# Performance work log

Measured on AMD Instinct MI355X. Metric: run time of the kernel, lower is better.

Reference implementation:

```python
import jax, jax.numpy as jnp
import numpy as np


def _wn(v, g):
    # weight-norm: w[o, i] = g[o] * v[o, i] / ||v[o, :]||
    return g[:, None] * v / jnp.linalg.norm(v, axis=1, keepdims=True)


def setup_inputs() -> dict:
    key = jax.random.key(0)
    ks = jax.random.split(key, 8)
    B, C, H, W = 16, 512, 64, 64
    K, D = 2048, 64
    return {
        "z": jax.random.normal(ks[0], (B, C, H, W), dtype=jnp.float32),
        "codebook": jax.random.normal(ks[1], (K, D), dtype=jnp.float32),
        "in_v": jax.random.normal(ks[2], (D, C), dtype=jnp.float32),
        "in_g": jax.random.uniform(ks[3], (D,), dtype=jnp.float32, minval=0.5, maxval=1.5),
        "in_b": jax.random.normal(ks[4], (D,), dtype=jnp.float32) * 0.02,
        "out_v": jax.random.normal(ks[5], (C, D), dtype=jnp.float32),
        "out_g": jax.random.uniform(ks[6], (C,), dtype=jnp.float32, minval=0.5, maxval=1.5),
        "out_b": jax.random.normal(ks[7], (C,), dtype=jnp.float32) * 0.02,
    }


def reference(z, codebook, in_v, in_g, in_b, out_v, out_g, out_b):
    COMMIT_W = 0.25
    B, C, H, W = z.shape
    D = codebook.shape[1]

    Wi = _wn(in_v, in_g)    # [D, C]
    Wo = _wn(out_v, out_g)  # [C, D]

    # in_proj (1x1 conv): b c h w -> b d h w
    z_e = jnp.einsum('bchw,dc->bdhw', z, Wi) + in_b[None, :, None, None]

    # flatten tokens: (b h w) d
    z_e_flat = z_e.transpose(0, 2, 3, 1).reshape(-1, D)

    dist = (jnp.sum(z_e_flat * z_e_flat, axis=1, keepdims=True)
            - 2.0 * z_e_flat @ codebook.T
            + jnp.sum(codebook * codebook, axis=1)[None, :])
    indices_flat = jnp.argmin(dist, axis=1)            # [(BHW)]
    indices = indices_flat.reshape(B, H, W)

    z_q_flat = codebook[indices_flat]                  # gather [(BHW), D]
    z_q = z_q_flat.reshape(B, H, W, D).transpose(0, 3, 1, 2)  # b d h w

    sg = jax.lax.stop_gradient
    commitment_loss = jnp.mean((sg(z_e) - z_q) ** 2)
    codebook_loss = jnp.mean((sg(z_q) - z_e) ** 2)
    vq_loss = codebook_loss + COMMIT_W * commitment_loss

    # straight-through
    z_q_st = z_e + sg(z_q - z_e)

    # out_proj (1x1 conv): b d h w -> b c h w
    out = jnp.einsum('bdhw,cd->bchw', z_q_st, Wo) + out_b[None, :, None, None]
    return out, indices, vq_loss
```

## Files before the change

### kernel.cpp

```cpp
#include <hip/hip_runtime.h>
#include <math.h>


typedef __attribute__((address_space(1))) const unsigned int* gas_ptr;
typedef __attribute__((address_space(3))) unsigned int* las_ptr;
#define GLD_LDS16(gsrc, ldst) \
  __builtin_amdgcn_global_load_lds((gas_ptr)(const void*)(gsrc), \
                                   (las_ptr)(void*)(ldst), 16, 0, 0)


__global__ void k_prep_wi(const float* __restrict__ v, const float* __restrict__ g,
                          float* __restrict__ wiT){
  const int d = blockIdx.x;
  const int tid = threadIdx.x;
  float s = 0.f;
  for (int c = tid; c < 512; c += 256){ float x = v[d*512+c]; s = fmaf(x,x,s); }
  __shared__ float red[4];
  #pragma unroll
  for (int o = 32; o > 0; o >>= 1) s += __shfl_down(s, o);
  if ((tid & 63) == 0) red[tid >> 6] = s;
  __syncthreads();
  const float nrm = sqrtf(red[0]+red[1]+red[2]+red[3]);
  const float gd = g[d];
  for (int c = tid; c < 512; c += 256) wiT[c*64 + d] = gd * v[d*512+c] / nrm;
}

__global__ void k_prep_wo(const float* __restrict__ v, const float* __restrict__ g,
                          float* __restrict__ wot){
  const int c = blockIdx.x;
  const int d = threadIdx.x;
  const float x = v[c*64+d];
  float s = x*x;
  #pragma unroll
  for (int o = 32; o > 0; o >>= 1) s += __shfl_down(s, o);
  const float nrm = __shfl(sqrtf(s), 0);
  wot[d*512 + c] = g[c] * x / nrm;
}

__global__ void k_table(const float* __restrict__ cbk, const float* __restrict__ wot,
                        const float* __restrict__ ob, float* __restrict__ table,
                        float* __restrict__ ne, float* __restrict__ cbm2T){
  const int k = blockIdx.x;
  const int tid = threadIdx.x;
  __shared__ float e[64];
  if (tid < 64) e[tid] = cbk[k*64 + tid];
  __syncthreads();
  if (tid < 64){
    float x = e[tid];
    cbm2T[tid*2048 + k] = -2.0f * x;
    float s = x*x;
    #pragma unroll
    for (int o = 32; o > 0; o >>= 1) s += __shfl_down(s, o);
    if (tid == 0) ne[k] = s;
  }
  const int c = tid;
  float acc = ob[c];
  #pragma unroll 16
  for (int d = 0; d < 64; d++) acc = fmaf(e[d], wot[d*512 + c], acc);
  table[(size_t)k*512 + c] = acc;
}

__global__ __launch_bounds__(256, 1) void k_inproj(
    const float* __restrict__ z, const float* __restrict__ wiT,
    const float* __restrict__ inb, float* __restrict__ ze)
{
  __shared__ __align__(16) float z_s[16*256];
  __shared__ __align__(16) float wi_s[16*68];
  const int tid = threadIdx.x;
  const int T0  = blockIdx.x << 8;
  const int b   = T0 >> 12;
  const int hw0 = T0 & 4095;
  const float* zb = z + ((size_t)b << 21) + hw0;

  const int tgp = tid & 31;
  const int dgp = tid >> 5;
  const int ccb = tid >> 6;
  const int c64 = tid & 63;

  float acc[8][8];
  #pragma unroll
  for (int i = 0; i < 8; i++)
    #pragma unroll
    for (int j = 0; j < 8; j++) acc[i][j] = 0.f;

  float4 pz[4]; float pw[4];
  #pragma unroll
  for (int q = 0; q < 4; q++){
    pz[q] = *(const float4*)(zb + (size_t)(ccb + 4*q) * 4096 + c64*4);
    pw[q] = wiT[(ccb + 4*q)*64 + c64];
  }
  #pragma unroll
  for (int q = 0; q < 4; q++){
    *(float4*)&z_s[(ccb + 4*q)*256 + c64*4] = pz[q];
    wi_s[(ccb + 4*q)*68 + c64] = pw[q];
  }
  __syncthreads();

  for (int c0 = 0;;){
    const int nxt = c0 + 16;
    if (nxt < 512){
      #pragma unroll
      for (int q = 0; q < 4; q++){
        pz[q] = *(const float4*)(zb + (size_t)(nxt + ccb + 4*q) * 4096 + c64*4);
        pw[q] = wiT[(nxt + ccb + 4*q)*64 + c64];
      }
    }
    #pragma unroll 4
    for (int cc = 0; cc < 16; cc++){
      const float4 ta = *(const float4*)&z_s[cc*256 + tgp*4];
      const float4 tb = *(const float4*)&z_s[cc*256 + 128 + tgp*4];
      const float4 w0 = *(const float4*)&wi_s[cc*68 + dgp*8];
      const float4 w1 = *(const float4*)&wi_s[cc*68 + dgp*8 + 4];
      const float tv[8] = {ta.x,ta.y,ta.z,ta.w, tb.x,tb.y,tb.z,tb.w};
      const float wv[8] = {w0.x,w0.y,w0.z,w0.w, w1.x,w1.y,w1.z,w1.w};
      #pragma unroll
      for (int i = 0; i < 8; i++)
        #pragma unroll
        for (int j = 0; j < 8; j++)
          acc[i][j] = fmaf(tv[j], wv[i], acc[i][j]);
    }
    if (nxt >= 512) break;
    __syncthreads();
    #pragma unroll
    for (int q = 0; q < 4; q++){
      *(float4*)&z_s[(ccb + 4*q)*256 + c64*4] = pz[q];
      wi_s[(ccb + 4*q)*68 + c64] = pw[q];
    }
    __syncthreads();
    c0 = nxt;
  }

  #pragma unroll
  for (int i = 0; i < 8; i++){
    const int d = dgp*8 + i;
    const float bd = inb[d];
    float4 o0 = {acc[i][0]+bd, acc[i][1]+bd, acc[i][2]+bd, acc[i][3]+bd};
    float4 o1 = {acc[i][4]+bd, acc[i][5]+bd, acc[i][6]+bd, acc[i][7]+bd};
    *(float4*)(ze + (size_t)d*65536 + T0 + tgp*4)       = o0;
    *(float4*)(ze + (size_t)d*65536 + T0 + 128 + tgp*4) = o1;
  }
}

__global__ __launch_bounds__(256, 2) void k_main3(
    const float* __restrict__ ze, const float* __restrict__ cbm2T,
    const float* __restrict__ cbk, const float* __restrict__ ne,
    const float* __restrict__ table, float* __restrict__ out,
    float* __restrict__ oidx, double* __restrict__ loss)
{
  __shared__ __align__(16) float ze_s[64*128];
  __shared__ __align__(16) float cb_s[2][8*272];
  __shared__ int bidx_s[128];

  const int tid = threadIdx.x;
  const int t0  = blockIdx.x << 7;
  const int b   = t0 >> 12;
  const int hw0 = t0 & 4095;
  const int w   = tid >> 6;
  const int l4  = (tid & 63) << 2;

  #pragma unroll
  for (int j = 0; j < 8; j++){
    const int idx = tid + 256*j;
    const int row = idx >> 5, col4 = idx & 31;
    *(float4*)&ze_s[row*128 + col4*4] =
        *(const float4*)(ze + (size_t)row*65536 + t0 + col4*4);
  }

  const int tg = tid & 15;
  const int kg = tid >> 4;
  float best[8]; int bidx[8];
  #pragma unroll
  for (int j = 0; j < 8; j++){ best[j] = INFINITY; bidx[j] = 0; }

  {
    const float* gb = cbm2T + (size_t)(2*w)*2048 + l4;
    GLD_LDS16(gb,        &cb_s[0][(2*w)  *272]);
    GLD_LDS16(gb + 2048, &cb_s[0][(2*w+1)*272]);
  }
  __syncthreads();

  float acc[8][16];
  for (int s = 0; s < 64; s++){
    const int buf = s & 1;
    const int dq = s & 7, kc = (s >> 3) << 8;
    if (s < 63){
      const int s1 = s + 1;
      const int ndq = s1 & 7, nkc = (s1 >> 3) << 8;
      const float* gb = cbm2T + (size_t)(ndq*8 + 2*w)*2048 + nkc + l4;
      GLD_LDS16(gb,        &cb_s[buf^1][(2*w)  *272]);
      GLD_LDS16(gb + 2048, &cb_s[buf^1][(2*w+1)*272]);
    }
    if (dq == 0){
      #pragma unroll
      for (int q = 0; q < 4; q++){
        const float4 nv = *(const float4*)&ne[kc + kg*16 + q*4];
        const float nn[4] = {nv.x, nv.y, nv.z, nv.w};
        #pragma unroll
        for (int r = 0; r < 4; r++)
          #pragma unroll
          for (int j = 0; j < 8; j++) acc[j][q*4+r] = nn[r];
      }
    }
    const int dbase = dq << 3;
    #pragma unroll
    for (int d = 0; d < 8; d++){
      const int dr = dbase + d;
      const float4 za = *(const float4*)&ze_s[dr*128 + tg*4];
      const float4 zb = *(const float4*)&ze_s[dr*128 + 64 + tg*4];
      const float4 c0 = *(const float4*)&cb_s[buf][d*272 + kg*16];
      const float4 c1 = *(const float4*)&cb_s[buf][d*272 + kg*16 + 4];
      const float4 c2 = *(const float4*)&cb_s[buf][d*272 + kg*16 + 8];
      const float4 c3 = *(const float4*)&cb_s[buf][d*272 + kg*16 + 12];
      const float zz[8]  = {za.x,za.y,za.z,za.w, zb.x,zb.y,zb.z,zb.w};
      const float cv[16] = {c0.x,c0.y,c0.z,c0.w, c1.x,c1.y,c1.z,c1.w,
                            c2.x,c2.y,c2.z,c2.w, c3.x,c3.y,c3.z,c3.w};
      #pragma unroll
      for (int j = 0; j < 8; j++)
        #pragma unroll
        for (int i = 0; i < 16; i++)
          acc[j][i] = fmaf(zz[j], cv[i], acc[j][i]);
    }
    if (dq == 7){
      #pragma unroll
      for (int i = 0; i < 16; i++){
        const int k = kc + kg*16 + i;
        #pragma unroll
        for (int j = 0; j < 8; j++)
          if (acc[j][i] < best[j]){ best[j] = acc[j][i]; bidx[j] = k; }
      }
    }
    __syncthreads();
  }

  float* rb = &cb_s[0][0];
  int*   ri = (int*)(&cb_s[0][0] + 2048);
  #pragma unroll
  for (int j = 0; j < 8; j++){
    const int t = (j < 4) ? (tg*4 + j) : (64 + tg*4 + (j - 4));
    rb[t*16 + kg] = best[j];
    ri[t*16 + kg] = bidx[j];
  }
  __syncthreads();

  float myloss = 0.f;
  if (tid < 128){
    const int t = tid;
    float bv = rb[t*16]; int bi = ri[t*16];
    #pragma unroll
    for (int q = 1; q < 16; q++){
      const float vq = rb[t*16 + q]; const int iq = ri[t*16 + q];
      if (vq < bv || (vq == bv && iq < bi)){ bv = vq; bi = iq; }
    }
    bidx_s[t] = bi;
    oidx[t0 + t] = (float)bi;
    const float* e = cbk + (size_t)bi * 64;
    #pragma unroll 8
    for (int d = 0; d < 64; d++){
      const float diff = ze_s[d*128 + t] - e[d];
      myloss = fmaf(diff, diff, myloss);
    }
  }
  #pragma unroll
  for (int o = 32; o > 0; o >>= 1) myloss += __shfl_down(myloss, o);
  if (tid < 128 && (tid & 63) == 0) atomicAdd(loss, (double)myloss);
  __syncthreads();

  {
    const int tl = tid & 127, cg = tid >> 7;
    const int myk = bidx_s[tl];
    const float* trow = table + ((size_t)myk << 9) + cg*256;
    float* ob = out + (((size_t)b) << 21) + hw0 + tl;
    #pragma unroll 4
    for (int ci = 0; ci < 64; ci++){
      const float4 v = *(const float4*)(trow + ci*4);
      const size_t cbase = (size_t)(cg*256 + ci*4) << 12;
      ob[cbase        ] = v.x;
      ob[cbase +  4096] = v.y;
      ob[cbase +  8192] = v.z;
      ob[cbase + 12288] = v.w;
    }
  }
}

__global__ void k_finish(const double* __restrict__ loss, float* __restrict__ oloss){
  *oloss = (float)(1.25 * (*loss) / 4194304.0);
}


extern "C" void kernel_launch(void* const* d_in, const int* in_sizes, int n_in,
                              void* d_out, int out_size, void* d_ws, size_t ws_size,
                              hipStream_t stream) {
  const float* z   = (const float*)d_in[0];
  const float* cbk = (const float*)d_in[1];
  const float* inv = (const float*)d_in[2];
  const float* ing = (const float*)d_in[3];
  const float* inb = (const float*)d_in[4];
  const float* ov  = (const float*)d_in[5];
  const float* og  = (const float*)d_in[6];
  const float* ob  = (const float*)d_in[7];

  float* ws    = (float*)d_ws;
  float* wiT   = ws;
  float* wot   = ws + 32768;
  float* table = ws + 65536;
  float* ne    = ws + 65536 + 1048576;
  double* loss = (double*)(ws + 1116160);
  float* cbm2T = ws + 1179648;
  float* zebuf = ws + 2097152;

  float* out   = (float*)d_out;
  float* oidx  = out + 33554432;
  float* oloss = out + 33619968;

  hipMemsetAsync(loss, 0, sizeof(double), stream);
  k_prep_wi<<<64, 256, 0, stream>>>(inv, ing, wiT);
  k_prep_wo<<<512, 64, 0, stream>>>(ov, og, wot);
  k_table<<<2048, 512, 0, stream>>>(cbk, wot, ob, table, ne, cbm2T);
  k_inproj<<<256, 256, 0, stream>>>(z, wiT, inb, zebuf);
  k_main3<<<512, 256, 0, stream>>>(zebuf, cbm2T, cbk, ne, table, out, oidx, loss);
  k_finish<<<1, 1, 0, stream>>>(loss, oloss);
}
```

Measured before the change: 348.2 us.

## Fuse in-projection into main VQ kernel with 64-token tiles

Merges the separate in-projection kernel into the distance/argmin/output kernel, so z_e is computed into shared memory per block instead of written to and reread from a global buffer. Tiles shrink from 128 to 64 tokens per block, with smaller accumulator arrays and a higher occupancy target (4 blocks per CU, 1024 blocks in total), and z/weight tiles are streamed through async global-to-LDS loads. The trade-off is that each block reloads the whole codebook for half as many tokens, doubling codebook traffic and per-token sync overhead.

```diff
diff --git a/kernel.cpp b/kernel.cpp
--- a/kernel.cpp
+++ b/kernel.cpp
@@ -60,135 +60,96 @@
   table[(size_t)k*512 + c] = acc;
 }
 
-__global__ __launch_bounds__(256, 1) void k_inproj(
+__global__ __launch_bounds__(256, 4) void k_main(
     const float* __restrict__ z, const float* __restrict__ wiT,
-    const float* __restrict__ inb, float* __restrict__ ze)
-{
-  __shared__ __align__(16) float z_s[16*256];
-  __shared__ __align__(16) float wi_s[16*68];
-  const int tid = threadIdx.x;
-  const int T0  = blockIdx.x << 8;
-  const int b   = T0 >> 12;
-  const int hw0 = T0 & 4095;
-  const float* zb = z + ((size_t)b << 21) + hw0;
-
-  const int tgp = tid & 31;
-  const int dgp = tid >> 5;
-  const int ccb = tid >> 6;
-  const int c64 = tid & 63;
-
-  float acc[8][8];
-  #pragma unroll
-  for (int i = 0; i < 8; i++)
-    #pragma unroll
-    for (int j = 0; j < 8; j++) acc[i][j] = 0.f;
-
-  float4 pz[4]; float pw[4];
-  #pragma unroll
-  for (int q = 0; q < 4; q++){
-    pz[q] = *(const float4*)(zb + (size_t)(ccb + 4*q) * 4096 + c64*4);
-    pw[q] = wiT[(ccb + 4*q)*64 + c64];
-  }
-  #pragma unroll
-  for (int q = 0; q < 4; q++){
-    *(float4*)&z_s[(ccb + 4*q)*256 + c64*4] = pz[q];
-    wi_s[(ccb + 4*q)*68 + c64] = pw[q];
-  }
-  __syncthreads();
-
-  for (int c0 = 0;;){
-    const int nxt = c0 + 16;
-    if (nxt < 512){
-      #pragma unroll
-      for (int q = 0; q < 4; q++){
-        pz[q] = *(const float4*)(zb + (size_t)(nxt + ccb + 4*q) * 4096 + c64*4);
-        pw[q] = wiT[(nxt + ccb + 4*q)*64 + c64];
-      }
-    }
-    #pragma unroll 4
-    for (int cc = 0; cc < 16; cc++){
-      const float4 ta = *(const float4*)&z_s[cc*256 + tgp*4];
-      const float4 tb = *(const float4*)&z_s[cc*256 + 128 + tgp*4];
-      const float4 w0 = *(const float4*)&wi_s[cc*68 + dgp*8];
-      const float4 w1 = *(const float4*)&wi_s[cc*68 + dgp*8 + 4];
-      const float tv[8] = {ta.x,ta.y,ta.z,ta.w, tb.x,tb.y,tb.z,tb.w};
-      const float wv[8] = {w0.x,w0.y,w0.z,w0.w, w1.x,w1.y,w1.z,w1.w};
-      #pragma unroll
-      for (int i = 0; i < 8; i++)
-        #pragma unroll
-        for (int j = 0; j < 8; j++)
-          acc[i][j] = fmaf(tv[j], wv[i], acc[i][j]);
-    }
-    if (nxt >= 512) break;
-    __syncthreads();
-    #pragma unroll
-    for (int q = 0; q < 4; q++){
-      *(float4*)&z_s[(ccb + 4*q)*256 + c64*4] = pz[q];
-      wi_s[(ccb + 4*q)*68 + c64] = pw[q];
-    }
-    __syncthreads();
-    c0 = nxt;
-  }
-
-  #pragma unroll
-  for (int i = 0; i < 8; i++){
-    const int d = dgp*8 + i;
-    const float bd = inb[d];
-    float4 o0 = {acc[i][0]+bd, acc[i][1]+bd, acc[i][2]+bd, acc[i][3]+bd};
-    float4 o1 = {acc[i][4]+bd, acc[i][5]+bd, acc[i][6]+bd, acc[i][7]+bd};
-    *(float4*)(ze + (size_t)d*65536 + T0 + tgp*4)       = o0;
-    *(float4*)(ze + (size_t)d*65536 + T0 + 128 + tgp*4) = o1;
-  }
-}
-
-__global__ __launch_bounds__(256, 2) void k_main3(
-    const float* __restrict__ ze, const float* __restrict__ cbm2T,
+    const float* __restrict__ inb, const float* __restrict__ cbm2T,
     const float* __restrict__ cbk, const float* __restrict__ ne,
     const float* __restrict__ table, float* __restrict__ out,
     float* __restrict__ oidx, double* __restrict__ loss)
 {
-  __shared__ __align__(16) float ze_s[64*128];
-  __shared__ __align__(16) float cb_s[2][8*272];
-  __shared__ int bidx_s[128];
-
-  const int tid = threadIdx.x;
-  const int t0  = blockIdx.x << 7;
-  const int b   = t0 >> 12;
-  const int hw0 = t0 & 4095;
-  const int w   = tid >> 6;
-  const int l4  = (tid & 63) << 2;
-
-  #pragma unroll
-  for (int j = 0; j < 8; j++){
-    const int idx = tid + 256*j;
-    const int row = idx >> 5, col4 = idx & 31;
-    *(float4*)&ze_s[row*128 + col4*4] =
-        *(const float4*)(ze + (size_t)row*65536 + t0 + col4*4);
-  }
-
-  const int tg = tid & 15;
-  const int kg = tid >> 4;
-  float best[8]; int bidx[8];
-  #pragma unroll
-  for (int j = 0; j < 8; j++){ best[j] = INFINITY; bidx[j] = 0; }
+  __shared__ __align__(16) float ze_s[64*68];
+  __shared__ __align__(16) float rgb[2*2176];
+  __shared__ int bidx_s[64];
+
+  const int tid  = threadIdx.x;
+  const int w    = tid >> 6;
+  const int lane = tid & 63;
+  const int t0   = blockIdx.x << 6;
+  const int b    = t0 >> 12;
+  const int hw0  = t0 & 4095;
+  const float* zb = z + ((size_t)b << 21) + hw0;
+
+  const int tg  = tid & 15;
+  const int dgp = tid >> 4;
+
+  const int srow = w*4 + (lane >> 4);
+  const int scol = (lane & 15) << 2;
+
+  float acc1[4][4];
+  #pragma unroll
+  for (int i = 0; i < 4; i++)
+    #pragma unroll
+    for (int j = 0; j < 4; j++) acc1[i][j] = 0.f;
+
+  GLD_LDS16(zb + (size_t)srow*4096 + scol,  &rgb[0*2176 + w*256]);
+  GLD_LDS16(wiT + srow*64 + scol,           &rgb[0*2176 + 1024 + w*256]);
+  __syncthreads();
+
+  for (int c = 0; c < 32; c++){
+    const int buf = c & 1;
+    if (c < 31){
+      const int c0n = (c+1) << 4;
+      GLD_LDS16(zb + (size_t)(c0n + srow)*4096 + scol, &rgb[(buf^1)*2176 + w*256]);
+      GLD_LDS16(wiT + (c0n + srow)*64 + scol,          &rgb[(buf^1)*2176 + 1024 + w*256]);
+    }
+    const float* zc = &rgb[buf*2176];
+    const float* wc = &rgb[buf*2176 + 1024];
+    #pragma unroll 4
+    for (int cc = 0; cc < 16; cc++){
+      const float4 ta = *(const float4*)&zc[cc*64 + tg*4];
+      const float4 wv = *(const float4*)&wc[cc*64 + dgp*4];
+      const float tv[4] = {ta.x, ta.y, ta.z, ta.w};
+      const float wvv[4] = {wv.x, wv.y, wv.z, wv.w};
+      #pragma unroll
+      for (int i = 0; i < 4; i++)
+        #pragma unroll
+        for (int j = 0; j < 4; j++)
+          acc1[i][j] = fmaf(tv[j], wvv[i], acc1[i][j]);
+    }
+    __syncthreads();
+  }
+
+  #pragma unroll
+  for (int i = 0; i < 4; i++){
+    const int d = dgp*4 + i;
+    const float bd = inb[d];
+    float4 o = {acc1[i][0]+bd, acc1[i][1]+bd, acc1[i][2]+bd, acc1[i][3]+bd};
+    *(float4*)&ze_s[d*68 + tg*4] = o;
+  }
+  __syncthreads();
+
+  const int kg = dgp;
+  float best[4]; int bidx[4];
+  #pragma unroll
+  for (int j = 0; j < 4; j++){ best[j] = INFINITY; bidx[j] = 0; }
 
   {
-    const float* gb = cbm2T + (size_t)(2*w)*2048 + l4;
-    GLD_LDS16(gb,        &cb_s[0][(2*w)  *272]);
-    GLD_LDS16(gb + 2048, &cb_s[0][(2*w+1)*272]);
-  }
-  __syncthreads();
-
-  float acc[8][16];
+    const float* gbs = cbm2T + (size_t)(2*w)*2048 + lane*4;
+    GLD_LDS16(gbs,        &rgb[0*2176 + (2*w)  *272]);
+    GLD_LDS16(gbs + 2048, &rgb[0*2176 + (2*w+1)*272]);
+  }
+  __syncthreads();
+
+  float acc[4][16];
   for (int s = 0; s < 64; s++){
     const int buf = s & 1;
     const int dq = s & 7, kc = (s >> 3) << 8;
     if (s < 63){
       const int s1 = s + 1;
       const int ndq = s1 & 7, nkc = (s1 >> 3) << 8;
-      const float* gb = cbm2T + (size_t)(ndq*8 + 2*w)*2048 + nkc + l4;
-      GLD_LDS16(gb,        &cb_s[buf^1][(2*w)  *272]);
-      GLD_LDS16(gb + 2048, &cb_s[buf^1][(2*w+1)*272]);
+      const float* gbs = cbm2T + (size_t)(ndq*8 + 2*w)*2048 + nkc + lane*4;
+      GLD_LDS16(gbs,        &rgb[(buf^1)*2176 + (2*w)  *272]);
+      GLD_LDS16(gbs + 2048, &rgb[(buf^1)*2176 + (2*w+1)*272]);
     }
     if (dq == 0){
       #pragma unroll
@@ -198,24 +159,24 @@
         #pragma unroll
         for (int r = 0; r < 4; r++)
           #pragma unroll
-          for (int j = 0; j < 8; j++) acc[j][q*4+r] = nn[r];
+          for (int j = 0; j < 4; j++) acc[j][q*4+r] = nn[r];
       }
     }
+    const float* cbf = &rgb[buf*2176];
     const int dbase = dq << 3;
     #pragma unroll
     for (int d = 0; d < 8; d++){
       const int dr = dbase + d;
-      const float4 za = *(const float4*)&ze_s[dr*128 + tg*4];
-      const float4 zb = *(const float4*)&ze_s[dr*128 + 64 + tg*4];
-      const float4 c0 = *(const float4*)&cb_s[buf][d*272 + kg*16];
-      const float4 c1 = *(const float4*)&cb_s[buf][d*272 + kg*16 + 4];
-      const float4 c2 = *(const float4*)&cb_s[buf][d*272 + kg*16 + 8];
-      const float4 c3 = *(const float4*)&cb_s[buf][d*272 + kg*16 + 12];
-      const float zz[8]  = {za.x,za.y,za.z,za.w, zb.x,zb.y,zb.z,zb.w};
+      const float4 za = *(const float4*)&ze_s[dr*68 + tg*4];
+      const float4 c0 = *(const float4*)&cbf[d*272 + kg*16];
+      const float4 c1 = *(const float4*)&cbf[d*272 + kg*16 + 4];
+      const float4 c2 = *(const float4*)&cbf[d*272 + kg*16 + 8];
+      const float4 c3 = *(const float4*)&cbf[d*272 + kg*16 + 12];
+      const float zz[4]  = {za.x, za.y, za.z, za.w};
       const float cv[16] = {c0.x,c0.y,c0.z,c0.w, c1.x,c1.y,c1.z,c1.w,
                             c2.x,c2.y,c2.z,c2.w, c3.x,c3.y,c3.z,c3.w};
       #pragma unroll
-      for (int j = 0; j < 8; j++)
+      for (int j = 0; j < 4; j++)
         #pragma unroll
         for (int i = 0; i < 16; i++)
           acc[j][i] = fmaf(zz[j], cv[i], acc[j][i]);
@@ -225,25 +186,24 @@
       for (int i = 0; i < 16; i++){
         const int k = kc + kg*16 + i;
         #pragma unroll
-        for (int j = 0; j < 8; j++)
+        for (int j = 0; j < 4; j++)
           if (acc[j][i] < best[j]){ best[j] = acc[j][i]; bidx[j] = k; }
       }
     }
     __syncthreads();
   }
 
-  float* rb = &cb_s[0][0];
-  int*   ri = (int*)(&cb_s[0][0] + 2048);
-  #pragma unroll
-  for (int j = 0; j < 8; j++){
-    const int t = (j < 4) ? (tg*4 + j) : (64 + tg*4 + (j - 4));
+  float* rb = rgb;
+  int*   ri = (int*)(rgb + 1024);
+  #pragma unroll
+  for (int j = 0; j < 4; j++){
+    const int t = tg*4 + j;
     rb[t*16 + kg] = best[j];
     ri[t*16 + kg] = bidx[j];
   }
   __syncthreads();
 
-  float myloss = 0.f;
-  if (tid < 128){
+  if (tid < 64){
     const int t = tid;
     float bv = rb[t*16]; int bi = ri[t*16];
     #pragma unroll
@@ -253,27 +213,28 @@
     }
     bidx_s[t] = bi;
     oidx[t0 + t] = (float)bi;
+    float myloss = 0.f;
     const float* e = cbk + (size_t)bi * 64;
     #pragma unroll 8
     for (int d = 0; d < 64; d++){
-      const float diff = ze_s[d*128 + t] - e[d];
+      const float diff = ze_s[d*68 + t] - e[d];
       myloss = fmaf(diff, diff, myloss);
     }
-  }
-  #pragma unroll
-  for (int o = 32; o > 0; o >>= 1) myloss += __shfl_down(myloss, o);
-  if (tid < 128 && (tid & 63) == 0) atomicAdd(loss, (double)myloss);
+    #pragma unroll
+    for (int o = 32; o > 0; o >>= 1) myloss += __shfl_down(myloss, o);
+    if (t == 0) atomicAdd(loss, (double)myloss);
+  }
   __syncthreads();
 
   {
-    const int tl = tid & 127, cg = tid >> 7;
+    const int tl = tid & 63, cg = tid >> 6;
     const int myk = bidx_s[tl];
-    const float* trow = table + ((size_t)myk << 9) + cg*256;
+    const float* trow = table + ((size_t)myk << 9) + cg*128;
     float* ob = out + (((size_t)b) << 21) + hw0 + tl;
     #pragma unroll 4
-    for (int ci = 0; ci < 64; ci++){
+    for (int ci = 0; ci < 32; ci++){
       const float4 v = *(const float4*)(trow + ci*4);
-      const size_t cbase = (size_t)(cg*256 + ci*4) << 12;
+      const size_t cbase = (size_t)(cg*128 + ci*4) << 12;
       ob[cbase        ] = v.x;
       ob[cbase +  4096] = v.y;
       ob[cbase +  8192] = v.z;
@@ -306,7 +267,6 @@
   float* ne    = ws + 65536 + 1048576;
   double* loss = (double*)(ws + 1116160);
   float* cbm2T = ws + 1179648;
-  float* zebuf = ws + 2097152;
 
   float* out   = (float*)d_out;
   float* oidx  = out + 33554432;
@@ -316,7 +276,6 @@
   k_prep_wi<<<64, 256, 0, stream>>>(inv, ing, wiT);
   k_prep_wo<<<512, 64, 0, stream>>>(ov, og, wot);
   k_table<<<2048, 512, 0, stream>>>(cbk, wot, ob, table, ne, cbm2T);
-  k_inproj<<<256, 256, 0, stream>>>(z, wiT, inb, zebuf);
-  k_main3<<<512, 256, 0, stream>>>(zebuf, cbm2T, cbk, ne, table, out, oidx, loss);
+  k_main<<<1024, 256, 0, stream>>>(z, wiT, inb, cbm2T, cbk, ne, table, out, oidx, loss);
   k_finish<<<1, 1, 0, stream>>>(loss, oloss);
 }
```

Result: slower. 385.7 us (+10.8%).

## Split codebook argmin into quarter-codebook scan blocks plus a merge kernel

Applied to the files above, without the earlier changes.

The fused distance/argmin/output kernel is replaced by two kernels. The first runs 4096 blocks, each holding a 512-entry quarter of the codebook in LDS and scanning 64 tokens, and writes a per-quarter best candidate. The second merges the four candidates, computes the loss, and scatters the precomputed output-table rows. The goal is more parallelism and less streaming of the codebook per block. In exchange it adds a kernel launch, candidate traffic through global memory, a large LDS footprint limiting occupancy to one block, and a re-read of z_e from global memory in the merge.

```diff
diff --git a/kernel.cpp b/kernel.cpp
--- a/kernel.cpp
+++ b/kernel.cpp
@@ -1,12 +1,6 @@
 #include <hip/hip_runtime.h>
 #include <math.h>
 
-
-typedef __attribute__((address_space(1))) const unsigned int* gas_ptr;
-typedef __attribute__((address_space(3))) unsigned int* las_ptr;
-#define GLD_LDS16(gsrc, ldst) \
-  __builtin_amdgcn_global_load_lds((gas_ptr)(const void*)(gsrc), \
-                                   (las_ptr)(void*)(ldst), 16, 0, 0)
 
 
 __global__ void k_prep_wi(const float* __restrict__ v, const float* __restrict__ g,
@@ -141,139 +135,154 @@
   }
 }
 
-__global__ __launch_bounds__(256, 2) void k_main3(
-    const float* __restrict__ ze, const float* __restrict__ cbm2T,
-    const float* __restrict__ cbk, const float* __restrict__ ne,
+__global__ __launch_bounds__(256, 1) void k_scan(
+    const float* __restrict__ zebuf, const float* __restrict__ cbm2T,
+    const float* __restrict__ ne, float* __restrict__ candv,
+    int* __restrict__ candi)
+{
+  __shared__ __align__(16) float cb_s[32*1044];
+  __shared__ __align__(16) float ze_s[64*68];
+  const int tid = threadIdx.x;
+  const int q  = blockIdx.x & 3;
+  const int t0 = (blockIdx.x >> 2) << 6;
+
+  {
+    const float* src = cbm2T + (q << 9);
+    for (int m = 0; m < 32; m++){
+      const int g = m*1024 + tid*4;
+      const int d = g >> 9, kcol = g & 511;
+      const float4 v = *(const float4*)(src + d*2048 + kcol);
+      *(float4*)&cb_s[(kcol >> 4)*1044 + d*16 + (kcol & 15)] = v;
+    }
+  }
+  {
+    const int r0 = tid >> 4, c4 = (tid & 15) << 2;
+    #pragma unroll
+    for (int m = 0; m < 4; m++){
+      const int d = r0 + m*16;
+      *(float4*)&ze_s[d*68 + c4] =
+          *(const float4*)(zebuf + (size_t)d*65536 + t0 + c4);
+    }
+  }
+  __syncthreads();
+
+  const int tg = tid & 7;
+  const int kg = tid >> 3;
+  const int kbase = (q << 9) + (kg << 4);
+
+  float acc[8][16];
+  #pragma unroll
+  for (int i4 = 0; i4 < 4; i4++){
+    const float4 nv = *(const float4*)&ne[kbase + i4*4];
+    #pragma unroll
+    for (int j = 0; j < 8; j++){
+      acc[j][i4*4  ] = nv.x; acc[j][i4*4+1] = nv.y;
+      acc[j][i4*4+2] = nv.z; acc[j][i4*4+3] = nv.w;
+    }
+  }
+
+#define P8(CV, I) \
+  acc[0][I]=fmaf(za.x ,CV,acc[0][I]); acc[1][I]=fmaf(za.y ,CV,acc[1][I]); \
+  acc[2][I]=fmaf(za.z ,CV,acc[2][I]); acc[3][I]=fmaf(za.w ,CV,acc[3][I]); \
+  acc[4][I]=fmaf(zb4.x,CV,acc[4][I]); acc[5][I]=fmaf(zb4.y,CV,acc[5][I]); \
+  acc[6][I]=fmaf(zb4.z,CV,acc[6][I]); acc[7][I]=fmaf(zb4.w,CV,acc[7][I]);
+
+  const float* cbr = &cb_s[kg*1044];
+  #pragma unroll 2
+  for (int d = 0; d < 64; d++){
+    const float4 za  = *(const float4*)&ze_s[d*68 + tg*8];
+    const float4 zb4 = *(const float4*)&ze_s[d*68 + tg*8 + 4];
+    const float4 c0 = *(const float4*)(cbr + d*16);
+    const float4 c1 = *(const float4*)(cbr + d*16 + 4);
+    const float4 c2 = *(const float4*)(cbr + d*16 + 8);
+    const float4 c3 = *(const float4*)(cbr + d*16 + 12);
+    P8(c0.x, 0)  P8(c0.y, 1)  P8(c0.z, 2)  P8(c0.w, 3)
+    P8(c1.x, 4)  P8(c1.y, 5)  P8(c1.z, 6)  P8(c1.w, 7)
+    P8(c2.x, 8)  P8(c2.y, 9)  P8(c2.z,10)  P8(c2.w,11)
+    P8(c3.x,12)  P8(c3.y,13)  P8(c3.z,14)  P8(c3.w,15)
+  }
+#undef P8
+
+  float best[8]; int bidx[8];
+  #pragma unroll
+  for (int j = 0; j < 8; j++){ best[j] = INFINITY; bidx[j] = 0; }
+  #pragma unroll
+  for (int i = 0; i < 16; i++){
+    const int k = kbase + i;
+    #pragma unroll
+    for (int j = 0; j < 8; j++)
+      if (acc[j][i] < best[j]){ best[j] = acc[j][i]; bidx[j] = k; }
+  }
+
+  __syncthreads();
+  float* rb = cb_s;
+  int*   ri = (int*)(cb_s + 2048);
+  #pragma unroll
+  for (int j = 0; j < 8; j++){
+    const int t = tg*8 + j;
+    rb[t*32 + kg] = best[j];
+    ri[t*32 + kg] = bidx[j];
+  }
+  __syncthreads();
+
+  if (tid < 64){
+    const int t = tid;
+    float bv = rb[t*32]; int bi = ri[t*32];
+    #pragma unroll
+    for (int kk = 1; kk < 32; kk++){
+      const float vq = rb[t*32 + kk]; const int iq = ri[t*32 + kk];
+      if (vq < bv || (vq == bv && iq < bi)){ bv = vq; bi = iq; }
+    }
+    candv[(q << 16) + t0 + t] = bv;
+    candi[(q << 16) + t0 + t] = bi;
+  }
+}
+
+__global__ __launch_bounds__(256) void k_merge(
+    const float* __restrict__ candv, const int* __restrict__ candi,
+    const float* __restrict__ zebuf, const float* __restrict__ cbk,
     const float* __restrict__ table, float* __restrict__ out,
     float* __restrict__ oidx, double* __restrict__ loss)
 {
-  __shared__ __align__(16) float ze_s[64*128];
-  __shared__ __align__(16) float cb_s[2][8*272];
-  __shared__ int bidx_s[128];
-
-  const int tid = threadIdx.x;
-  const int t0  = blockIdx.x << 7;
+  __shared__ int bidx_s[64];
+  const int tid = threadIdx.x;
+  const int t0  = blockIdx.x << 6;
   const int b   = t0 >> 12;
   const int hw0 = t0 & 4095;
-  const int w   = tid >> 6;
-  const int l4  = (tid & 63) << 2;
-
-  #pragma unroll
-  for (int j = 0; j < 8; j++){
-    const int idx = tid + 256*j;
-    const int row = idx >> 5, col4 = idx & 31;
-    *(float4*)&ze_s[row*128 + col4*4] =
-        *(const float4*)(ze + (size_t)row*65536 + t0 + col4*4);
-  }
-
-  const int tg = tid & 15;
-  const int kg = tid >> 4;
-  float best[8]; int bidx[8];
-  #pragma unroll
-  for (int j = 0; j < 8; j++){ best[j] = INFINITY; bidx[j] = 0; }
-
-  {
-    const float* gb = cbm2T + (size_t)(2*w)*2048 + l4;
-    GLD_LDS16(gb,        &cb_s[0][(2*w)  *272]);
-    GLD_LDS16(gb + 2048, &cb_s[0][(2*w+1)*272]);
-  }
-  __syncthreads();
-
-  float acc[8][16];
-  for (int s = 0; s < 64; s++){
-    const int buf = s & 1;
-    const int dq = s & 7, kc = (s >> 3) << 8;
-    if (s < 63){
-      const int s1 = s + 1;
-      const int ndq = s1 & 7, nkc = (s1 >> 3) << 8;
-      const float* gb = cbm2T + (size_t)(ndq*8 + 2*w)*2048 + nkc + l4;
-      GLD_LDS16(gb,        &cb_s[buf^1][(2*w)  *272]);
-      GLD_LDS16(gb + 2048, &cb_s[buf^1][(2*w+1)*272]);
-    }
-    if (dq == 0){
-      #pragma unroll
-      for (int q = 0; q < 4; q++){
-        const float4 nv = *(const float4*)&ne[kc + kg*16 + q*4];
-        const float nn[4] = {nv.x, nv.y, nv.z, nv.w};
-        #pragma unroll
-        for (int r = 0; r < 4; r++)
-          #pragma unroll
-          for (int j = 0; j < 8; j++) acc[j][q*4+r] = nn[r];
-      }
-    }
-    const int dbase = dq << 3;
-    #pragma unroll
-    for (int d = 0; d < 8; d++){
-      const int dr = dbase + d;
-      const float4 za = *(const float4*)&ze_s[dr*128 + tg*4];
-      const float4 zb = *(const float4*)&ze_s[dr*128 + 64 + tg*4];
-      const float4 c0 = *(const float4*)&cb_s[buf][d*272 + kg*16];
-      const float4 c1 = *(const float4*)&cb_s[buf][d*272 + kg*16 + 4];
-      const float4 c2 = *(const float4*)&cb_s[buf][d*272 + kg*16 + 8];
-      const float4 c3 = *(const float4*)&cb_s[buf][d*272 + kg*16 + 12];
-      const float zz[8]  = {za.x,za.y,za.z,za.w, zb.x,zb.y,zb.z,zb.w};
-      const float cv[16] = {c0.x,c0.y,c0.z,c0.w, c1.x,c1.y,c1.z,c1.w,
-                            c2.x,c2.y,c2.z,c2.w, c3.x,c3.y,c3.z,c3.w};
-      #pragma unroll
-      for (int j = 0; j < 8; j++)
-        #pragma unroll
-        for (int i = 0; i < 16; i++)
-          acc[j][i] = fmaf(zz[j], cv[i], acc[j][i]);
-    }
-    if (dq == 7){
-      #pragma unroll
-      for (int i = 0; i < 16; i++){
-        const int k = kc + kg*16 + i;
-        #pragma unroll
-        for (int j = 0; j < 8; j++)
-          if (acc[j][i] < best[j]){ best[j] = acc[j][i]; bidx[j] = k; }
-      }
-    }
-    __syncthreads();
-  }
-
-  float* rb = &cb_s[0][0];
-  int*   ri = (int*)(&cb_s[0][0] + 2048);
-  #pragma unroll
-  for (int j = 0; j < 8; j++){
-    const int t = (j < 4) ? (tg*4 + j) : (64 + tg*4 + (j - 4));
-    rb[t*16 + kg] = best[j];
-    ri[t*16 + kg] = bidx[j];
-  }
-  __syncthreads();
-
-  float myloss = 0.f;
-  if (tid < 128){
+
+  if (tid < 64){
     const int t = tid;
-    float bv = rb[t*16]; int bi = ri[t*16];
-    #pragma unroll
-    for (int q = 1; q < 16; q++){
-      const float vq = rb[t*16 + q]; const int iq = ri[t*16 + q];
-      if (vq < bv || (vq == bv && iq < bi)){ bv = vq; bi = iq; }
+    float bv = candv[t0 + t]; int bi = candi[t0 + t];
+    #pragma unroll
+    for (int qq = 1; qq < 4; qq++){
+      const float vq = candv[(qq << 16) + t0 + t];
+      const int   iq = candi[(qq << 16) + t0 + t];
+      if (vq < bv){ bv = vq; bi = iq; }
     }
     bidx_s[t] = bi;
     oidx[t0 + t] = (float)bi;
+    float myloss = 0.f;
     const float* e = cbk + (size_t)bi * 64;
     #pragma unroll 8
     for (int d = 0; d < 64; d++){
-      const float diff = ze_s[d*128 + t] - e[d];
+      const float diff = zebuf[(size_t)d*65536 + t0 + t] - e[d];
       myloss = fmaf(diff, diff, myloss);
     }
-  }
-  #pragma unroll
-  for (int o = 32; o > 0; o >>= 1) myloss += __shfl_down(myloss, o);
-  if (tid < 128 && (tid & 63) == 0) atomicAdd(loss, (double)myloss);
+    #pragma unroll
+    for (int o = 32; o > 0; o >>= 1) myloss += __shfl_down(myloss, o);
+    if (t == 0) atomicAdd(loss, (double)myloss);
+  }
   __syncthreads();
 
   {
-    const int tl = tid & 127, cg = tid >> 7;
+    const int tl = tid & 63, cg = tid >> 6;
     const int myk = bidx_s[tl];
-    const float* trow = table + ((size_t)myk << 9) + cg*256;
+    const float* trow = table + ((size_t)myk << 9) + cg*128;
     float* ob = out + (((size_t)b) << 21) + hw0 + tl;
     #pragma unroll 4
-    for (int ci = 0; ci < 64; ci++){
+    for (int ci = 0; ci < 32; ci++){
       const float4 v = *(const float4*)(trow + ci*4);
-      const size_t cbase = (size_t)(cg*256 + ci*4) << 12;
+      const size_t cbase = (size_t)(cg*128 + ci*4) << 12;
       ob[cbase        ] = v.x;
       ob[cbase +  4096] = v.y;
       ob[cbase +  8192] = v.z;
@@ -303,10 +312,12 @@
   float* wiT   = ws;
   float* wot   = ws + 32768;
   float* table = ws + 65536;
-  float* ne    = ws + 65536 + 1048576;
+  float* ne    = ws + 1114112;
   double* loss = (double*)(ws + 1116160);
   float* cbm2T = ws + 1179648;
   float* zebuf = ws + 2097152;
+  float* candv = ws + 6291456;
+  int*   candi = (int*)(ws + 6553600);
 
   float* out   = (float*)d_out;
   float* oidx  = out + 33554432;
@@ -317,6 +328,7 @@
   k_prep_wo<<<512, 64, 0, stream>>>(ov, og, wot);
   k_table<<<2048, 512, 0, stream>>>(cbk, wot, ob, table, ne, cbm2T);
   k_inproj<<<256, 256, 0, stream>>>(z, wiT, inb, zebuf);
-  k_main3<<<512, 256, 0, stream>>>(zebuf, cbm2T, cbk, ne, table, out, oidx, loss);
+  k_scan<<<4096, 256, 0, stream>>>(zebuf, cbm2T, ne, candv, candi);
+  k_merge<<<1024, 256, 0, stream>>>(candv, candi, zebuf, cbk, table, out, oidx, loss);
   k_finish<<<1, 1, 0, stream>>>(loss, oloss);
 }
```

After: 496.5 us. +42.6%, slower.

## Deepen codebook prefetch to distance two with one barrier per step

Applied to the files above, without the earlier changes.

The main distance kernel now uses four LDS buffers for codebook slices and prefetches two steps ahead. It uses explicit vmcnt waits with a single raw s_barrier per step in place of the trailing __syncthreads. The codebook norms are staged into LDS once instead of being read from global memory each chunk, and the FMA loop runs at raised wave priority. The aim is to hide global-to-LDS latency and cut barrier stalls, at the cost of more LDS per block (which may affect occupancy) and hand-tuned waitcnt logic that must stay in step with the outstanding loads.

```diff
diff --git a/kernel.cpp b/kernel.cpp
--- a/kernel.cpp
+++ b/kernel.cpp
@@ -141,14 +141,15 @@
   }
 }
 
-__global__ __launch_bounds__(256, 2) void k_main3(
+__global__ __launch_bounds__(256, 2) void k_main4(
     const float* __restrict__ ze, const float* __restrict__ cbm2T,
     const float* __restrict__ cbk, const float* __restrict__ ne,
     const float* __restrict__ table, float* __restrict__ out,
     float* __restrict__ oidx, double* __restrict__ loss)
 {
   __shared__ __align__(16) float ze_s[64*128];
-  __shared__ __align__(16) float cb_s[2][8*272];
+  __shared__ __align__(16) float cb_s[4][8*272];
+  __shared__ __align__(16) float ne_s[2048];
   __shared__ int bidx_s[128];
 
   const int tid = threadIdx.x;
@@ -172,28 +173,43 @@
   #pragma unroll
   for (int j = 0; j < 8; j++){ best[j] = INFINITY; bidx[j] = 0; }
 
+  GLD_LDS16(ne + w*512 + l4,        &ne_s[w*512]);
+  GLD_LDS16(ne + w*512 + 256 + l4,  &ne_s[w*512 + 256]);
   {
     const float* gb = cbm2T + (size_t)(2*w)*2048 + l4;
     GLD_LDS16(gb,        &cb_s[0][(2*w)  *272]);
     GLD_LDS16(gb + 2048, &cb_s[0][(2*w+1)*272]);
   }
+  {
+    const float* gb = cbm2T + (size_t)(1*8 + 2*w)*2048 + l4;
+    GLD_LDS16(gb,        &cb_s[1][(2*w)  *272]);
+    GLD_LDS16(gb + 2048, &cb_s[1][(2*w+1)*272]);
+  }
   __syncthreads();
 
   float acc[8][16];
   for (int s = 0; s < 64; s++){
-    const int buf = s & 1;
+    const int buf = s & 3;
     const int dq = s & 7, kc = (s >> 3) << 8;
-    if (s < 63){
-      const int s1 = s + 1;
-      const int ndq = s1 & 7, nkc = (s1 >> 3) << 8;
+    if (s < 62){
+      const int s2 = s + 2;
+      const int ndq = s2 & 7, nkc = (s2 >> 3) << 8;
       const float* gb = cbm2T + (size_t)(ndq*8 + 2*w)*2048 + nkc + l4;
-      GLD_LDS16(gb,        &cb_s[buf^1][(2*w)  *272]);
-      GLD_LDS16(gb + 2048, &cb_s[buf^1][(2*w+1)*272]);
-    }
+      GLD_LDS16(gb,        &cb_s[s2 & 3][(2*w)  *272]);
+      GLD_LDS16(gb + 2048, &cb_s[s2 & 3][(2*w+1)*272]);
+      asm volatile("s_waitcnt vmcnt(4)" ::: "memory");
+    } else if (s == 62){
+      asm volatile("s_waitcnt vmcnt(2)" ::: "memory");
+    } else {
+      asm volatile("s_waitcnt vmcnt(0)" ::: "memory");
+    }
+    __builtin_amdgcn_s_barrier();
+    __builtin_amdgcn_sched_barrier(0);
+
     if (dq == 0){
       #pragma unroll
       for (int q = 0; q < 4; q++){
-        const float4 nv = *(const float4*)&ne[kc + kg*16 + q*4];
+        const float4 nv = *(const float4*)&ne_s[kc + kg*16 + q*4];
         const float nn[4] = {nv.x, nv.y, nv.z, nv.w};
         #pragma unroll
         for (int r = 0; r < 4; r++)
@@ -202,6 +218,7 @@
       }
     }
     const int dbase = dq << 3;
+    __builtin_amdgcn_s_setprio(1);
     #pragma unroll
     for (int d = 0; d < 8; d++){
       const int dr = dbase + d;
@@ -220,6 +237,7 @@
         for (int i = 0; i < 16; i++)
           acc[j][i] = fmaf(zz[j], cv[i], acc[j][i]);
     }
+    __builtin_amdgcn_s_setprio(0);
     if (dq == 7){
       #pragma unroll
       for (int i = 0; i < 16; i++){
@@ -229,8 +247,8 @@
           if (acc[j][i] < best[j]){ best[j] = acc[j][i]; bidx[j] = k; }
       }
     }
-    __syncthreads();
-  }
+  }
+  __syncthreads();
 
   float* rb = &cb_s[0][0];
   int*   ri = (int*)(&cb_s[0][0] + 2048);
@@ -303,7 +321,7 @@
   float* wiT   = ws;
   float* wot   = ws + 32768;
   float* table = ws + 65536;
-  float* ne    = ws + 65536 + 1048576;
+  float* ne    = ws + 1114112;
   double* loss = (double*)(ws + 1116160);
   float* cbm2T = ws + 1179648;
   float* zebuf = ws + 2097152;
@@ -317,6 +335,6 @@
   k_prep_wo<<<512, 64, 0, stream>>>(ov, og, wot);
   k_table<<<2048, 512, 0, stream>>>(cbk, wot, ob, table, ne, cbm2T);
   k_inproj<<<256, 256, 0, stream>>>(z, wiT, inb, zebuf);
-  k_main3<<<512, 256, 0, stream>>>(zebuf, cbm2T, cbk, ne, table, out, oidx, loss);
+  k_main4<<<512, 256, 0, stream>>>(zebuf, cbm2T, cbk, ne, table, out, oidx, loss);
   k_finish<<<1, 1, 0, stream>>>(loss, oloss);
 }
```

New measurement: 988.9 us. 2.84x slower.
